# Kernel optimization log

Measured on AMD Instinct MI355X. Metric: run time of the kernel, lower is better.

The kernel has to match this reference:

```python
import jax, jax.numpy as jnp
import numpy as np
from jax import lax

V, H, B, S, N, E = 32000, 128, 8, 512, 50000, 600000


def lstm(x, W_ih, W_hh, b):
    # x: [B,T,D]; W_ih: [4H,D]; W_hh: [4H,H]; b: [4H] (b_ih+b_hh combined)
    Bsz = x.shape[0]
    Hd = W_hh.shape[1]
    xg = jnp.einsum('btd,gd->btg', x, W_ih) + b  # precompute input gates [B,T,4H]
    h0 = jnp.zeros((Bsz, Hd), x.dtype)
    c0 = jnp.zeros((Bsz, Hd), x.dtype)

    def step(carry, g_t):
        h, c = carry
        g = g_t + h @ W_hh.T
        i, f, gg, o = jnp.split(g, 4, axis=-1)
        i = jax.nn.sigmoid(i)
        f = jax.nn.sigmoid(f)
        gg = jnp.tanh(gg)
        o = jax.nn.sigmoid(o)
        c = f * c + i * gg
        h = o * jnp.tanh(c)
        return (h, c), h

    _, hs = lax.scan(step, (h0, c0), jnp.swapaxes(xg, 0, 1))
    return jnp.swapaxes(hs, 0, 1)  # [B,T,H]


def gcn_conv(x, W, b, src, dst, n_nodes):
    # PyG GCNConv: add self-loops, symmetric normalization, out = A_hat (x W) + b
    h = x @ W.T  # [N,H]
    deg = jax.ops.segment_sum(jnp.ones(src.shape[0], x.dtype), dst, num_segments=n_nodes) + 1.0
    dinv = lax.rsqrt(deg)
    norm = dinv[src] * dinv[dst]  # [E]
    agg = jax.ops.segment_sum(h[src] * norm[:, None], dst, num_segments=n_nodes)
    agg = agg + h * (dinv * dinv)[:, None]  # self-loop contribution
    return agg + b


def setup_inputs() -> dict:
    key = jax.random.key(0)
    ks = jax.random.split(key, 20)
    s = 0.02
    return {
        'json_input': jax.random.randint(ks[0], (B, S), 0, V, dtype=jnp.int32),
        'node_ids': jax.random.randint(ks[1], (N,), 0, V, dtype=jnp.int32),
        'edge_index': jax.random.randint(ks[2], (2, E), 0, N, dtype=jnp.int32),
        'embedding': jax.random.normal(ks[3], (V, H), jnp.float32) * s,
        'W_ih_enc': jax.random.normal(ks[4], (4 * H, H), jnp.float32) * s,
        'W_hh_enc': jax.random.normal(ks[5], (4 * H, H), jnp.float32) * s,
        'b_enc': jnp.zeros((4 * H,), jnp.float32),
        'W1': jax.random.normal(ks[6], (H, H), jnp.float32) * s,
        'b1': jnp.zeros((H,), jnp.float32),
        'W2': jax.random.normal(ks[7], (H, H), jnp.float32) * s,
        'b2': jnp.zeros((H,), jnp.float32),
        'Wf': jax.random.normal(ks[8], (H, 2 * H), jnp.float32) * s,
        'bf': jnp.zeros((H,), jnp.float32),
        'W_ih_dec': jax.random.normal(ks[9], (4 * H, H), jnp.float32) * s,
        'W_hh_dec': jax.random.normal(ks[10], (4 * H, H), jnp.float32) * s,
        'b_dec': jnp.zeros((4 * H,), jnp.float32),
        'Wo': jax.random.normal(ks[11], (V, H), jnp.float32) * s,
        'bo': jnp.zeros((V,), jnp.float32),
    }


def reference(json_input, node_ids, edge_index, embedding, W_ih_enc, W_hh_enc, b_enc,
              W1, b1, W2, b2, Wf, bf, W_ih_dec, W_hh_dec, b_dec, Wo, bo):
    src, dst = edge_index[0], edge_index[1]
    # sequence branch
    json_emb = embedding[json_input]                      # [B,S,H]
    json_encoded = lstm(json_emb, W_ih_enc, W_hh_enc, b_enc)  # [B,S,H]
    # graph branch
    node_x = embedding[node_ids]                          # [N,H]
    x = gcn_conv(node_x, W1, b1, src, dst, node_ids.shape[0])
    x = gcn_conv(x, W2, b2, src, dst, node_ids.shape[0])
    # fusion
    graph_summary = jnp.broadcast_to(x.mean(axis=0, keepdims=True), (json_encoded.shape[0], x.shape[1]))
    combined = jnp.concatenate([json_encoded.mean(axis=1), graph_summary], axis=1)  # [B,2H]
    fused = combined @ Wf.T + bf                          # [B,H]
    fused_seq = jnp.broadcast_to(fused[:, None, :], (fused.shape[0], json_input.shape[1], fused.shape[1]))
    # decode
    decoded = lstm(fused_seq, W_ih_dec, W_hh_dec, b_dec)  # [B,S,H]
    return decoded @ Wo.T + bo                            # [B,S,V]
```

## Files before the change

kernel.cpp:

```cpp
#include <hip/hip_runtime.h>
#include <hip/hip_bf16.h>
#include <stdint.h>

#define VV 32000
#define HH 128
#define BB 8
#define SS 512
#define NNODE 50000
#define NEDGE 600000

typedef __attribute__((ext_vector_type(8))) short s16x8;
typedef __attribute__((ext_vector_type(4))) float f32x4;

__global__ __launch_bounds__(256) void xg_enc_kernel(
    const int* __restrict__ jin, const float* __restrict__ emb,
    const float* __restrict__ Wih, const float* __restrict__ bvec,
    float* __restrict__ xg)
{
  __shared__ __align__(16) float arow[8][128];
  const int tid = threadIdx.x, blk = blockIdx.x;
  {
    int r = tid >> 5, c = (tid & 31) << 2;
    int tok = jin[blk*8 + r];
    *(float4*)&arow[r][c] = *(const float4*)&emb[(size_t)tok*HH + c];
  }
  __syncthreads();
  const int g0 = tid * 2;
  const float* w0 = Wih + (size_t)g0*HH;
  const float* w1 = w0 + HH;
  float acc0[8], acc1[8];
  #pragma unroll
  for (int r=0;r<8;r++){ acc0[r]=0.f; acc1[r]=0.f; }
  for (int k=0;k<HH;k+=4) {
    float4 wa = *(const float4*)&w0[k];
    float4 wb = *(const float4*)&w1[k];
    #pragma unroll
    for (int r=0;r<8;r++) {
      float4 av = *(const float4*)&arow[r][k];
      acc0[r] += av.x*wa.x + av.y*wa.y + av.z*wa.z + av.w*wa.w;
      acc1[r] += av.x*wb.x + av.y*wb.y + av.z*wb.z + av.w*wb.w;
    }
  }
  float bb0 = bvec[g0], bb1 = bvec[g0+1];
  #pragma unroll
  for (int r=0;r<8;r++) {
    size_t row = (size_t)blk*8 + r;
    xg[row*512 + g0]     = acc0[r] + bb0;
    xg[row*512 + g0 + 1] = acc1[r] + bb1;
  }
}

__global__ __launch_bounds__(512, 2) void enc_scan_kernel(
    const float* __restrict__ xg, const float* __restrict__ Whh,
    float* __restrict__ hmean)
{
  __shared__ __align__(16) float h_s[128];
  __shared__ float act_s[512];
  const int b = blockIdx.x, tid = threadIdx.x;

  const f32x4* Wrow = (const f32x4*)(Whh + (size_t)tid*HH);
  f32x4 w[32];
  #pragma unroll
  for (int k=0;k<32;k++) w[k] = Wrow[k];
  #pragma unroll
  for (int k=0;k<32;k++) asm volatile("" : "+v"(w[k]));

  const float* xgrow = xg + (size_t)b*SS*512;
  float xv = xgrow[tid];
  if (tid < 128) h_s[tid] = 0.f;
  float cstate = 0.f, hsum = 0.f;
  __syncthreads();

  for (int t=0;t<SS;t++) {
    int tn = (t < SS-1) ? (t+1) : t;
    float nxv = xgrow[(size_t)tn*512 + tid];
    float a0=0.f,a1=0.f,a2=0.f,a3=0.f;
    #pragma unroll
    for (int k=0;k<32;k++) {
      f32x4 hv = *(const f32x4*)&h_s[k*4];
      a0 += w[k].x*hv.x; a1 += w[k].y*hv.y;
      a2 += w[k].z*hv.z; a3 += w[k].w*hv.w;
    }
    float s = (a0+a1)+(a2+a3) + xv;
    int gid = tid >> 7;
    float act = (gid==2) ? tanhf(s) : 1.0f/(1.0f+expf(-s));
    act_s[tid] = act;
    __syncthreads();
    if (tid < 128) {
      float i_ = act_s[tid], f_ = act_s[128+tid], g_ = act_s[256+tid], o_ = act_s[384+tid];
      cstate = f_*cstate + i_*g_;
      float hh = o_*tanhf(cstate);
      h_s[tid] = hh;
      hsum += hh;
    }
    xv = nxv;
    __syncthreads();
  }
  if (tid < 128) hmean[b*HH + tid] = hsum * (1.0f/512.0f);
}

__global__ __launch_bounds__(512) void dec_gemm_kernel(
    const float* __restrict__ xgdec, const float* __restrict__ Whh,
    __hip_bfloat16* __restrict__ ahi, __hip_bfloat16* __restrict__ alo,
    const __hip_bfloat16* __restrict__ Bhi, const __hip_bfloat16* __restrict__ Blo,
    const float* __restrict__ bo, float* __restrict__ out, int* __restrict__ prog)
{
  __shared__ __align__(16) char shraw[131072];
  const int bid = blockIdx.x, tid = threadIdx.x;

  if (bid < 8) {
    float* h_s   = (float*)shraw;
    float* act_s = ((float*)shraw) + 128;
    const int b = bid;

    const f32x4* Wrow = (const f32x4*)(Whh + (size_t)tid*HH);
    f32x4 w[32];
    #pragma unroll
    for (int k=0;k<32;k++) w[k] = Wrow[k];
    #pragma unroll
    for (int k=0;k<32;k++) asm volatile("" : "+v"(w[k]));

    float xv = xgdec[b*512 + tid];
    if (tid < 128) h_s[tid] = 0.f;
    float cstate = 0.f;
    __syncthreads();

    for (int t=0;t<SS;t++) {
      float a0=0.f,a1=0.f,a2=0.f,a3=0.f;
      #pragma unroll
      for (int k=0;k<32;k++) {
        f32x4 hv = *(const f32x4*)&h_s[k*4];
        a0 += w[k].x*hv.x; a1 += w[k].y*hv.y;
        a2 += w[k].z*hv.z; a3 += w[k].w*hv.w;
      }
      float s = (a0+a1)+(a2+a3) + xv;
      int gid = tid >> 7;
      float act = (gid==2) ? tanhf(s) : 1.0f/(1.0f+expf(-s));
      act_s[tid] = act;
      __syncthreads();
      if (tid < 128) {
        float i_ = act_s[tid], f_ = act_s[128+tid], g_ = act_s[256+tid], o_ = act_s[384+tid];
        cstate = f_*cstate + i_*g_;
        float hh = o_*tanhf(cstate);
        h_s[tid] = hh;
        size_t row = (size_t)b*SS + t;
        __hip_bfloat16 hi = __float2bfloat16(hh);
        float rem = hh - __bfloat162float(hi);
        ahi[row*HH + tid] = hi;
        alo[row*HH + tid] = __float2bfloat16(rem);
      }
      __syncthreads();
      if ((t & 127) == 127) {
        __threadfence();
        __syncthreads();
        if (tid == 0)
          __hip_atomic_store(&prog[b*32], (t >> 7) + 1,
                             __ATOMIC_RELEASE, __HIP_MEMORY_SCOPE_AGENT);
      }
    }
  } else {
    short* smem = (short*)shraw;
    const int gbid = bid - 8;
    const int c    = gbid / 1000;
    const int r    = gbid % 1000;
    const int b    = r / 125;
    const int nblk = r % 125;
    const int mtile = b*4 + c;

    if (tid == 0) {
      while (__hip_atomic_load(&prog[b*32], __ATOMIC_ACQUIRE,
                               __HIP_MEMORY_SCOPE_AGENT) <= c)
        __builtin_amdgcn_s_sleep(64);
    }
    __syncthreads();

    const short* bsrc[2] = {
      (const short*)Bhi + (size_t)nblk*256*HH,
      (const short*)Blo + (size_t)nblk*256*HH };
    #pragma unroll
    for (int p=0;p<2;p++) {
      #pragma unroll
      for (int it=0; it<8; it++) {
        int off  = it*8192 + tid*16;
        int row  = off >> 8;
        int soff = off ^ ((row & 15) << 4);
        __builtin_amdgcn_global_load_lds(
          (const __attribute__((address_space(1))) void*)((const char*)bsrc[p] + soff),
          (__attribute__((address_space(3))) void*)((char*)smem + p*65536 + off),
          16, 0, 0);
      }
    }
    __syncthreads();

    const int lane = tid & 63;
    const int wid  = tid >> 6;
    const int wm = wid >> 2, wn = wid & 3;
    const int l15 = lane & 15, l4 = lane >> 4;
    const int mbase = mtile*128 + wm*64;
    const short* Ah = (const short*)ahi;
    const short* Al = (const short*)alo;

    f32x4 acc[4][4] = {};
    #pragma unroll
    for (int s=0;s<4;s++) {
      s16x8 bh[4], bl[4], ah[4], al[4];
      #pragma unroll
      for (int qn=0;qn<4;qn++) {
        int rb   = wn*64 + qn*16 + l15;
        int offb = (rb*256 + s*64 + l4*16) ^ ((rb & 15) << 4);
        bh[qn] = *(const s16x8*)((const char*)smem + offb);
        bl[qn] = *(const s16x8*)((const char*)smem + 65536 + offb);
      }
      #pragma unroll
      for (int qm=0;qm<4;qm++) {
        int arow = mbase + qm*16 + l15;
        size_t aoff = (size_t)arow*HH + s*32 + l4*8;
        ah[qm] = *(const s16x8*)(Ah + aoff);
        al[qm] = *(const s16x8*)(Al + aoff);
      }
      #pragma unroll
      for (int qm=0;qm<4;qm++) {
        #pragma unroll
        for (int qn=0;qn<4;qn++) {
          acc[qm][qn] = __builtin_amdgcn_mfma_f32_16x16x32_bf16(bh[qn], ah[qm], acc[qm][qn], 0,0,0);
          acc[qm][qn] = __builtin_amdgcn_mfma_f32_16x16x32_bf16(bl[qn], ah[qm], acc[qm][qn], 0,0,0);
          acc[qm][qn] = __builtin_amdgcn_mfma_f32_16x16x32_bf16(bh[qn], al[qm], acc[qm][qn], 0,0,0);
        }
      }
    }
    #pragma unroll
    for (int qm=0;qm<4;qm++) {
      int row = mbase + qm*16 + l15;
      #pragma unroll
      for (int qn=0;qn<4;qn++) {
        int colb = nblk*256 + wn*64 + qn*16 + l4*4;
        f32x4 bv = *(const f32x4*)&bo[colb];
        f32x4 o = acc[qm][qn] + bv;
        *(f32x4*)&out[(size_t)row*VV + colb] = o;
      }
    }
  }
}

__global__ __launch_bounds__(256) void edge_deg_kernel(const int* __restrict__ dst, float* __restrict__ deg) {
  int i = blockIdx.x*256 + threadIdx.x;
  if (i < NEDGE) atomicAdd(&deg[dst[i]], 1.0f);
}
__global__ __launch_bounds__(256) void node_dinv_kernel(const float* __restrict__ deg, float* __restrict__ dinv) {
  int n = blockIdx.x*256 + threadIdx.x;
  if (n < NNODE) dinv[n] = 1.0f / sqrtf(deg[n] + 1.0f);
}
__global__ __launch_bounds__(256) void edge_s1_kernel(const int* __restrict__ src, const int* __restrict__ dst,
    const float* __restrict__ dinv, float* __restrict__ s1) {
  int i = blockIdx.x*256 + threadIdx.x;
  if (i < NEDGE) atomicAdd(&s1[src[i]], dinv[dst[i]]);
}
__global__ __launch_bounds__(256) void node_c_kernel(const float* __restrict__ dinv, const float* __restrict__ s1,
    float* __restrict__ cc, float* __restrict__ csum) {
  __shared__ float red[256];
  int tid = threadIdx.x;
  int n = blockIdx.x*256 + tid;
  float v = 0.f;
  if (n < NNODE) { float d = dinv[n]; v = d*s1[n] + d*d; cc[n] = v; }
  red[tid] = v; __syncthreads();
  for (int sfl=128; sfl>0; sfl>>=1) { if (tid < sfl) red[tid] += red[tid+sfl]; __syncthreads(); }
  if (tid==0) atomicAdd(csum, red[0]);
}
__global__ __launch_bounds__(256) void edge_s2_kernel(const int* __restrict__ src, const int* __restrict__ dst,
    const float* __restrict__ dinv, const float* __restrict__ cc, float* __restrict__ s2) {
  int i = blockIdx.x*256 + threadIdx.x;
  if (i < NEDGE) { int d = dst[i]; atomicAdd(&s2[src[i]], cc[d]*dinv[d]); }
}
__global__ __launch_bounds__(256) void node_e_kernel(const float* __restrict__ dinv, const float* __restrict__ s2,
    const float* __restrict__ cc, float* __restrict__ ee) {
  int n = blockIdx.x*256 + threadIdx.x;
  if (n < NNODE) { float d = dinv[n]; ee[n] = d*s2[n] + cc[n]*d*d; }
}
__global__ __launch_bounds__(256) void gvec_kernel(const int* __restrict__ nids, const float* __restrict__ emb,
    const float* __restrict__ ee, float* __restrict__ gvec) {
  __shared__ float red[256];
  int tid = threadIdx.x;
  int j = tid & 127, sub = tid >> 7;
  float acc = 0.f;
  for (int n = blockIdx.x*2 + sub; n < NNODE; n += gridDim.x*2) {
    acc += ee[n] * emb[(size_t)nids[n]*HH + j];
  }
  red[tid] = acc; __syncthreads();
  if (tid < 128) atomicAdd(&gvec[j], red[tid] + red[tid+128]);
}
__global__ void graph_final_kernel(const float* __restrict__ gvec, const float* __restrict__ csum,
    const float* __restrict__ W1, const float* __restrict__ b1,
    const float* __restrict__ W2, const float* __restrict__ b2, float* __restrict__ mvec) {
  __shared__ float gs[128], v1[128];
  int j = threadIdx.x;
  gs[j] = gvec[j];
  __syncthreads();
  float a = 0.f;
  for (int k=0;k<128;k++) a += gs[k]*W1[j*128+k];
  v1[j] = a + csum[0]*b1[j];
  __syncthreads();
  float a2 = 0.f;
  for (int k=0;k<128;k++) a2 += v1[k]*W2[j*128+k];
  mvec[j] = a2 * (1.0f/(float)NNODE) + b2[j];
}

__global__ __launch_bounds__(512) void fusion_kernel(const float* __restrict__ hmean, const float* __restrict__ mvec,
    const float* __restrict__ Wf, const float* __restrict__ bfv,
    const float* __restrict__ Wihd, const float* __restrict__ bd, float* __restrict__ xgdec)
{
  __shared__ float comb[256];
  __shared__ float fus[128];
  int b = blockIdx.x, tid = threadIdx.x;
  if (tid < 128) comb[tid] = hmean[b*128 + tid];
  else if (tid < 256) comb[tid] = mvec[tid - 128];
  __syncthreads();
  if (tid < 128) {
    float a = 0.f;
    for (int k=0;k<256;k++) a += comb[k]*Wf[tid*256+k];
    fus[tid] = a + bfv[tid];
  }
  __syncthreads();
  float a = 0.f;
  for (int k=0;k<128;k++) a += fus[k]*Wihd[tid*128+k];
  xgdec[b*512 + tid] = a + bd[tid];
}

__global__ __launch_bounds__(256) void split_bf16_kernel(const float* __restrict__ x,
    __hip_bfloat16* __restrict__ hi, __hip_bfloat16* __restrict__ lo, int n4) {
  int i = blockIdx.x*256 + threadIdx.x;
  if (i >= n4) return;
  float4 v = *(const float4*)&x[i*4];
  float vv[4] = {v.x, v.y, v.z, v.w};
  #pragma unroll
  for (int k=0;k<4;k++) {
    __hip_bfloat16 h = __float2bfloat16(vv[k]);
    hi[i*4+k] = h;
    lo[i*4+k] = __float2bfloat16(vv[k] - __bfloat162float(h));
  }
}

extern "C" void kernel_launch(void* const* d_in, const int* in_sizes, int n_in,
                              void* d_out, int out_size, void* d_ws, size_t ws_size,
                              hipStream_t stream)
{
  (void)in_sizes; (void)n_in; (void)out_size; (void)ws_size;
  const int*   jin   = (const int*)d_in[0];
  const int*   nids  = (const int*)d_in[1];
  const int*   esrc  = (const int*)d_in[2];
  const int*   edst  = esrc + NEDGE;
  const float* emb   = (const float*)d_in[3];
  const float* WihE  = (const float*)d_in[4];
  const float* WhhE  = (const float*)d_in[5];
  const float* bE    = (const float*)d_in[6];
  const float* W1    = (const float*)d_in[7];
  const float* b1    = (const float*)d_in[8];
  const float* W2    = (const float*)d_in[9];
  const float* b2    = (const float*)d_in[10];
  const float* Wf    = (const float*)d_in[11];
  const float* bfv   = (const float*)d_in[12];
  const float* WihD  = (const float*)d_in[13];
  const float* WhhD  = (const float*)d_in[14];
  const float* bD    = (const float*)d_in[15];
  const float* Wo    = (const float*)d_in[16];
  const float* bo    = (const float*)d_in[17];
  float* out = (float*)d_out;

  char* ws = (char*)d_ws;
  size_t off = 0;
  auto alloc = [&](size_t bytes) { size_t o = off; off = (off + bytes + 255) & ~(size_t)255; return o; };

  int*   prog = (int*)(ws + alloc(BB*32*4));
  float* deg  = (float*)(ws + alloc(NNODE*4));
  float* s1   = (float*)(ws + alloc(NNODE*4));
  float* s2   = (float*)(ws + alloc(NNODE*4));
  float* gvec = (float*)(ws + alloc(128*4));
  float* csum = (float*)(ws + alloc(4));
  size_t zero_bytes = off;
  float* dinv = (float*)(ws + alloc(NNODE*4));
  float* cc   = (float*)(ws + alloc(NNODE*4));
  float* ee   = (float*)(ws + alloc(NNODE*4));
  float* mvec = (float*)(ws + alloc(128*4));
  float* hmean= (float*)(ws + alloc(BB*HH*4));
  float* xgdec= (float*)(ws + alloc(BB*512*4));
  float* xgenc= (float*)(ws + alloc((size_t)BB*SS*512*4));
  __hip_bfloat16* Ahi = (__hip_bfloat16*)(ws + alloc((size_t)BB*SS*HH*2));
  __hip_bfloat16* Alo = (__hip_bfloat16*)(ws + alloc((size_t)BB*SS*HH*2));
  __hip_bfloat16* Bhi = (__hip_bfloat16*)(ws + alloc((size_t)VV*HH*2));
  __hip_bfloat16* Blo = (__hip_bfloat16*)(ws + alloc((size_t)VV*HH*2));

  hipMemsetAsync(ws, 0, zero_bytes, stream);

  split_bf16_kernel<<<dim3((VV*HH/4+255)/256), dim3(256), 0, stream>>>(Wo, Bhi, Blo, VV*HH/4);

  xg_enc_kernel<<<dim3((BB*SS)/8), dim3(256), 0, stream>>>(jin, emb, WihE, bE, xgenc);
  enc_scan_kernel<<<dim3(BB), dim3(512), 0, stream>>>(xgenc, WhhE, hmean);

  edge_deg_kernel<<<dim3((NEDGE+255)/256), dim3(256), 0, stream>>>(edst, deg);
  node_dinv_kernel<<<dim3((NNODE+255)/256), dim3(256), 0, stream>>>(deg, dinv);
  edge_s1_kernel<<<dim3((NEDGE+255)/256), dim3(256), 0, stream>>>(esrc, edst, dinv, s1);
  node_c_kernel<<<dim3((NNODE+255)/256), dim3(256), 0, stream>>>(dinv, s1, cc, csum);
  edge_s2_kernel<<<dim3((NEDGE+255)/256), dim3(256), 0, stream>>>(esrc, edst, dinv, cc, s2);
  node_e_kernel<<<dim3((NNODE+255)/256), dim3(256), 0, stream>>>(dinv, s2, cc, ee);
  gvec_kernel<<<dim3(256), dim3(256), 0, stream>>>(nids, emb, ee, gvec);
  graph_final_kernel<<<dim3(1), dim3(128), 0, stream>>>(gvec, csum, W1, b1, W2, b2, mvec);

  fusion_kernel<<<dim3(BB), dim3(512), 0, stream>>>(hmean, mvec, Wf, bfv, WihD, bD, xgdec);
  dec_gemm_kernel<<<dim3(8 + 4000), dim3(512), 0, stream>>>(
      xgdec, WhhD, Ahi, Alo, Bhi, Blo, bo, out, prog);
}
```

Baseline: 1.284 ms.

## Fuse front-end kernels into one persistent kernel overlapping encoder scan with graph work

Replaces the encoder input-gate GEMM, encoder scan, Wo bf16 split and all GCN reduction kernels with one persistent launch. Eight blocks run the encoder scans while 240 worker blocks produce xg chunks, signalled through per-chunk counters, then do the bf16 split and graph stages separated by a software grid barrier. This overlaps the serial scan with the parallel work and removes many launches. The decoder GEMM also drops to 64-row M tiles with progress flags every 64 steps so projection starts earlier, at the cost of twice as many blocks. The software grid barrier relies on all 248 blocks being co-resident, which is a deadlock risk if they are not.

```diff
diff --git a/kernel.cpp b/kernel.cpp
--- a/kernel.cpp
+++ b/kernel.cpp
@@ -8,95 +8,198 @@
 #define SS 512
 #define NNODE 50000
 #define NEDGE 600000
+#define NWORK 240
 
 typedef __attribute__((ext_vector_type(8))) short s16x8;
 typedef __attribute__((ext_vector_type(4))) float f32x4;
 
-__global__ __launch_bounds__(256) void xg_enc_kernel(
-    const int* __restrict__ jin, const float* __restrict__ emb,
-    const float* __restrict__ Wih, const float* __restrict__ bvec,
-    float* __restrict__ xg)
-{
-  __shared__ __align__(16) float arow[8][128];
-  const int tid = threadIdx.x, blk = blockIdx.x;
-  {
-    int r = tid >> 5, c = (tid & 31) << 2;
-    int tok = jin[blk*8 + r];
-    *(float4*)&arow[r][c] = *(const float4*)&emb[(size_t)tok*HH + c];
+__device__ __forceinline__ void workers_barrier(int* bar, int tid) {
+  __syncthreads();
+  if (tid == 0) {
+    int g = __hip_atomic_load(&bar[32], __ATOMIC_ACQUIRE, __HIP_MEMORY_SCOPE_AGENT);
+    int old = __hip_atomic_fetch_add(&bar[0], 1, __ATOMIC_ACQ_REL, __HIP_MEMORY_SCOPE_AGENT);
+    if (old == NWORK-1) {
+      __hip_atomic_store(&bar[0], 0, __ATOMIC_RELAXED, __HIP_MEMORY_SCOPE_AGENT);
+      __hip_atomic_store(&bar[32], g+1, __ATOMIC_RELEASE, __HIP_MEMORY_SCOPE_AGENT);
+    } else {
+      while (__hip_atomic_load(&bar[32], __ATOMIC_ACQUIRE, __HIP_MEMORY_SCOPE_AGENT) == g)
+        __builtin_amdgcn_s_sleep(32);
+    }
   }
   __syncthreads();
-  const int g0 = tid * 2;
-  const float* w0 = Wih + (size_t)g0*HH;
-  const float* w1 = w0 + HH;
-  float acc0[8], acc1[8];
-  #pragma unroll
-  for (int r=0;r<8;r++){ acc0[r]=0.f; acc1[r]=0.f; }
-  for (int k=0;k<HH;k+=4) {
-    float4 wa = *(const float4*)&w0[k];
-    float4 wb = *(const float4*)&w1[k];
-    #pragma unroll
-    for (int r=0;r<8;r++) {
-      float4 av = *(const float4*)&arow[r][k];
-      acc0[r] += av.x*wa.x + av.y*wa.y + av.z*wa.z + av.w*wa.w;
-      acc1[r] += av.x*wb.x + av.y*wb.y + av.z*wb.z + av.w*wb.w;
+}
+
+__global__ __launch_bounds__(512) void front_kernel(
+    const int* __restrict__ jin, const float* __restrict__ emb,
+    const float* __restrict__ WihE, const float* __restrict__ bE,
+    float* xg, const float* __restrict__ WhhE, float* __restrict__ hmean,
+    const float* __restrict__ Wo, __hip_bfloat16* __restrict__ Bhi, __hip_bfloat16* __restrict__ Blo,
+    const int* __restrict__ esrc, const int* __restrict__ edst, const int* __restrict__ nids,
+    float* __restrict__ deg, float* __restrict__ dinv, float* __restrict__ s1,
+    float* __restrict__ s2, float* __restrict__ cc, float* __restrict__ ee,
+    float* __restrict__ csum, float* __restrict__ gvec,
+    const float* __restrict__ W1, const float* __restrict__ b1,
+    const float* __restrict__ W2, const float* __restrict__ b2, float* __restrict__ mvec,
+    int* ucnt, int* bar)
+{
+  __shared__ __align__(16) char shraw[131072];
+  const int bid = blockIdx.x, tid = threadIdx.x;
+
+  if (bid < 8) {
+    float* h_s   = (float*)shraw;
+    float* act_s = ((float*)shraw) + 128;
+    const int b = bid;
+
+    const f32x4* Wrow = (const f32x4*)(WhhE + (size_t)tid*HH);
+    f32x4 w[32];
+    #pragma unroll
+    for (int k=0;k<32;k++) w[k] = Wrow[k];
+    #pragma unroll
+    for (int k=0;k<32;k++) asm volatile("" : "+v"(w[k]));
+
+    const float* xgrow = xg + (size_t)b*SS*512;
+    if (tid == 0) {
+      while (__hip_atomic_load(&ucnt[(b*8+0)*32], __ATOMIC_ACQUIRE, __HIP_MEMORY_SCOPE_AGENT) < 8)
+        __builtin_amdgcn_s_sleep(16);
+    }
+    __syncthreads();
+    float xv = xgrow[tid];
+    if (tid < 128) h_s[tid] = 0.f;
+    float cstate = 0.f, hsum = 0.f;
+    __syncthreads();
+
+    for (int t=0;t<SS;t++) {
+      if ((t & 63) == 0) {
+        int cn = (t >> 6) + 1; if (cn > 7) cn = 7;
+        if (tid == 0) {
+          while (__hip_atomic_load(&ucnt[(b*8+cn)*32], __ATOMIC_ACQUIRE, __HIP_MEMORY_SCOPE_AGENT) < 8)
+            __builtin_amdgcn_s_sleep(16);
+        }
+        __syncthreads();
+      }
+      int tn = (t < SS-1) ? (t+1) : t;
+      float nxv = xgrow[(size_t)tn*512 + tid];
+      float a0=0.f,a1=0.f,a2=0.f,a3=0.f;
+      #pragma unroll
+      for (int k=0;k<32;k++) {
+        f32x4 hv = *(const f32x4*)&h_s[k*4];
+        a0 += w[k].x*hv.x; a1 += w[k].y*hv.y;
+        a2 += w[k].z*hv.z; a3 += w[k].w*hv.w;
+      }
+      float s = (a0+a1)+(a2+a3) + xv;
+      int gid = tid >> 7;
+      float act = (gid==2) ? tanhf(s) : 1.0f/(1.0f+expf(-s));
+      act_s[tid] = act;
+      __syncthreads();
+      if (tid < 128) {
+        float i_ = act_s[tid], f_ = act_s[128+tid], g_ = act_s[256+tid], o_ = act_s[384+tid];
+        cstate = f_*cstate + i_*g_;
+        float hh = o_*tanhf(cstate);
+        h_s[tid] = hh;
+        hsum += hh;
+      }
+      xv = nxv;
+      __syncthreads();
+    }
+    if (tid < 128) hmean[b*HH + tid] = hsum * (1.0f/512.0f);
+  } else {
+    const int wbid = bid - 8;
+    float (*arow)[128] = (float(*)[128])shraw;
+    float* red = (float*)(shraw + 8*128*4);
+
+    for (int u = wbid; u < 512; u += NWORK) {
+      int c = u >> 6, r2 = u & 63, b = r2 >> 3, sub = r2 & 7;
+      int row0 = b*512 + c*64 + sub*8;
+      if (tid < 256) {
+        int r = tid >> 5, c4 = (tid & 31) << 2;
+        int tok = jin[row0 + r];
+        *(float4*)&arow[r][c4] = *(const float4*)&emb[(size_t)tok*HH + c4];
+      }
+      __syncthreads();
+      const float* w0 = WihE + (size_t)tid*HH;
+      float acc[8];
+      #pragma unroll
+      for (int r=0;r<8;r++) acc[r] = 0.f;
+      for (int k=0;k<HH;k+=4) {
+        float4 wa = *(const float4*)&w0[k];
+        #pragma unroll
+        for (int r=0;r<8;r++) {
+          float4 av = *(const float4*)&arow[r][k];
+          acc[r] += av.x*wa.x + av.y*wa.y + av.z*wa.z + av.w*wa.w;
+        }
+      }
+      float bb = bE[tid];
+      #pragma unroll
+      for (int r=0;r<8;r++)
+        xg[(size_t)(row0+r)*512 + tid] = acc[r] + bb;
+      __threadfence();
+      __syncthreads();
+      if (tid == 0)
+        __hip_atomic_fetch_add(&ucnt[(b*8+c)*32], 1, __ATOMIC_RELEASE, __HIP_MEMORY_SCOPE_AGENT);
+      __syncthreads();
+    }
+    for (int i = wbid*512 + tid; i < VV*HH/4; i += NWORK*512) {
+      float4 v = *(const float4*)&Wo[i*4];
+      float vv[4] = {v.x, v.y, v.z, v.w};
+      #pragma unroll
+      for (int k=0;k<4;k++) {
+        __hip_bfloat16 h = __float2bfloat16(vv[k]);
+        Bhi[i*4+k] = h;
+        Blo[i*4+k] = __float2bfloat16(vv[k] - __bfloat162float(h));
+      }
+    }
+    workers_barrier(bar, tid);
+    for (int i = wbid*512 + tid; i < NEDGE; i += NWORK*512)
+      atomicAdd(&deg[edst[i]], 1.0f);
+    workers_barrier(bar, tid);
+    for (int n = wbid*512 + tid; n < NNODE; n += NWORK*512)
+      dinv[n] = 1.0f / sqrtf(deg[n] + 1.0f);
+    workers_barrier(bar, tid);
+    for (int i = wbid*512 + tid; i < NEDGE; i += NWORK*512)
+      atomicAdd(&s1[esrc[i]], dinv[edst[i]]);
+    workers_barrier(bar, tid);
+    {
+      float lsum = 0.f;
+      for (int n = wbid*512 + tid; n < NNODE; n += NWORK*512) {
+        float d = dinv[n]; float v = d*s1[n] + d*d; cc[n] = v; lsum += v;
+      }
+      red[tid] = lsum; __syncthreads();
+      for (int sfl=256; sfl>0; sfl>>=1) { if (tid < sfl) red[tid] += red[tid+sfl]; __syncthreads(); }
+      if (tid==0) atomicAdd(csum, red[0]);
+    }
+    workers_barrier(bar, tid);
+    for (int i = wbid*512 + tid; i < NEDGE; i += NWORK*512) {
+      int d = edst[i]; atomicAdd(&s2[esrc[i]], cc[d]*dinv[d]);
+    }
+    workers_barrier(bar, tid);
+    for (int n = wbid*512 + tid; n < NNODE; n += NWORK*512) {
+      float d = dinv[n]; ee[n] = d*s2[n] + cc[n]*d*d;
+    }
+    workers_barrier(bar, tid);
+    {
+      int j = tid & 127, sub = tid >> 7;
+      float acc = 0.f;
+      for (int n = wbid*4 + sub; n < NNODE; n += NWORK*4)
+        acc += ee[n] * emb[(size_t)nids[n]*HH + j];
+      red[tid] = acc; __syncthreads();
+      if (tid < 128) atomicAdd(&gvec[j], red[tid] + red[tid+128] + red[tid+256] + red[tid+384]);
+    }
+    workers_barrier(bar, tid);
+    if (wbid == 0 && tid < 128) {
+      float* gs = (float*)shraw;
+      float* v1 = gs + 128;
+      int j = tid;
+      gs[j] = gvec[j];
+      __builtin_amdgcn_s_barrier();
+      float a = 0.f;
+      for (int k=0;k<128;k++) a += gs[k]*W1[j*128+k];
+      v1[j] = a + csum[0]*b1[j];
+      __builtin_amdgcn_s_barrier();
+      float a2 = 0.f;
+      for (int k=0;k<128;k++) a2 += v1[k]*W2[j*128+k];
+      mvec[j] = a2 * (1.0f/(float)NNODE) + b2[j];
     }
   }
-  float bb0 = bvec[g0], bb1 = bvec[g0+1];
-  #pragma unroll
-  for (int r=0;r<8;r++) {
-    size_t row = (size_t)blk*8 + r;
-    xg[row*512 + g0]     = acc0[r] + bb0;
-    xg[row*512 + g0 + 1] = acc1[r] + bb1;
-  }
-}
-
-__global__ __launch_bounds__(512, 2) void enc_scan_kernel(
-    const float* __restrict__ xg, const float* __restrict__ Whh,
-    float* __restrict__ hmean)
-{
-  __shared__ __align__(16) float h_s[128];
-  __shared__ float act_s[512];
-  const int b = blockIdx.x, tid = threadIdx.x;
-
-  const f32x4* Wrow = (const f32x4*)(Whh + (size_t)tid*HH);
-  f32x4 w[32];
-  #pragma unroll
-  for (int k=0;k<32;k++) w[k] = Wrow[k];
-  #pragma unroll
-  for (int k=0;k<32;k++) asm volatile("" : "+v"(w[k]));
-
-  const float* xgrow = xg + (size_t)b*SS*512;
-  float xv = xgrow[tid];
-  if (tid < 128) h_s[tid] = 0.f;
-  float cstate = 0.f, hsum = 0.f;
-  __syncthreads();
-
-  for (int t=0;t<SS;t++) {
-    int tn = (t < SS-1) ? (t+1) : t;
-    float nxv = xgrow[(size_t)tn*512 + tid];
-    float a0=0.f,a1=0.f,a2=0.f,a3=0.f;
-    #pragma unroll
-    for (int k=0;k<32;k++) {
-      f32x4 hv = *(const f32x4*)&h_s[k*4];
-      a0 += w[k].x*hv.x; a1 += w[k].y*hv.y;
-      a2 += w[k].z*hv.z; a3 += w[k].w*hv.w;
-    }
-    float s = (a0+a1)+(a2+a3) + xv;
-    int gid = tid >> 7;
-    float act = (gid==2) ? tanhf(s) : 1.0f/(1.0f+expf(-s));
-    act_s[tid] = act;
-    __syncthreads();
-    if (tid < 128) {
-      float i_ = act_s[tid], f_ = act_s[128+tid], g_ = act_s[256+tid], o_ = act_s[384+tid];
-      cstate = f_*cstate + i_*g_;
-      float hh = o_*tanhf(cstate);
-      h_s[tid] = hh;
-      hsum += hh;
-    }
-    xv = nxv;
-    __syncthreads();
-  }
-  if (tid < 128) hmean[b*HH + tid] = hsum * (1.0f/512.0f);
 }
 
 __global__ __launch_bounds__(512) void dec_gemm_kernel(
@@ -150,11 +253,11 @@
         alo[row*HH + tid] = __float2bfloat16(rem);
       }
       __syncthreads();
-      if ((t & 127) == 127) {
+      if ((t & 63) == 63) {
         __threadfence();
         __syncthreads();
         if (tid == 0)
-          __hip_atomic_store(&prog[b*32], (t >> 7) + 1,
+          __hip_atomic_store(&prog[b*32], (t >> 6) + 1,
                              __ATOMIC_RELEASE, __HIP_MEMORY_SCOPE_AGENT);
       }
     }
@@ -165,7 +268,7 @@
     const int r    = gbid % 1000;
     const int b    = r / 125;
     const int nblk = r % 125;
-    const int mtile = b*4 + c;
+    const int mbase0 = b*512 + c*64;
 
     if (tid == 0) {
       while (__hip_atomic_load(&prog[b*32], __ATOMIC_ACQUIRE,
@@ -196,14 +299,14 @@
     const int wid  = tid >> 6;
     const int wm = wid >> 2, wn = wid & 3;
     const int l15 = lane & 15, l4 = lane >> 4;
-    const int mbase = mtile*128 + wm*64;
+    const int mbase = mbase0 + wm*32;
     const short* Ah = (const short*)ahi;
     const short* Al = (const short*)alo;
 
-    f32x4 acc[4][4] = {};
+    f32x4 acc[2][4] = {};
     #pragma unroll
     for (int s=0;s<4;s++) {
-      s16x8 bh[4], bl[4], ah[4], al[4];
+      s16x8 bh[4], bl[4], ah[2], al[2];
       #pragma unroll
       for (int qn=0;qn<4;qn++) {
         int rb   = wn*64 + qn*16 + l15;
@@ -212,14 +315,14 @@
         bl[qn] = *(const s16x8*)((const char*)smem + 65536 + offb);
       }
       #pragma unroll
-      for (int qm=0;qm<4;qm++) {
+      for (int qm=0;qm<2;qm++) {
         int arow = mbase + qm*16 + l15;
         size_t aoff = (size_t)arow*HH + s*32 + l4*8;
         ah[qm] = *(const s16x8*)(Ah + aoff);
         al[qm] = *(const s16x8*)(Al + aoff);
       }
       #pragma unroll
-      for (int qm=0;qm<4;qm++) {
+      for (int qm=0;qm<2;qm++) {
         #pragma unroll
         for (int qn=0;qn<4;qn++) {
           acc[qm][qn] = __builtin_amdgcn_mfma_f32_16x16x32_bf16(bh[qn], ah[qm], acc[qm][qn], 0,0,0);
@@ -229,7 +332,7 @@
       }
     }
     #pragma unroll
-    for (int qm=0;qm<4;qm++) {
+    for (int qm=0;qm<2;qm++) {
       int row = mbase + qm*16 + l15;
       #pragma unroll
       for (int qn=0;qn<4;qn++) {
@@ -240,68 +343,6 @@
       }
     }
   }
-}
-
-__global__ __launch_bounds__(256) void edge_deg_kernel(const int* __restrict__ dst, float* __restrict__ deg) {
-  int i = blockIdx.x*256 + threadIdx.x;
-  if (i < NEDGE) atomicAdd(&deg[dst[i]], 1.0f);
-}
-__global__ __launch_bounds__(256) void node_dinv_kernel(const float* __restrict__ deg, float* __restrict__ dinv) {
-  int n = blockIdx.x*256 + threadIdx.x;
-  if (n < NNODE) dinv[n] = 1.0f / sqrtf(deg[n] + 1.0f);
-}
-__global__ __launch_bounds__(256) void edge_s1_kernel(const int* __restrict__ src, const int* __restrict__ dst,
-    const float* __restrict__ dinv, float* __restrict__ s1) {
-  int i = blockIdx.x*256 + threadIdx.x;
-  if (i < NEDGE) atomicAdd(&s1[src[i]], dinv[dst[i]]);
-}
-__global__ __launch_bounds__(256) void node_c_kernel(const float* __restrict__ dinv, const float* __restrict__ s1,
-    float* __restrict__ cc, float* __restrict__ csum) {
-  __shared__ float red[256];
-  int tid = threadIdx.x;
-  int n = blockIdx.x*256 + tid;
-  float v = 0.f;
-  if (n < NNODE) { float d = dinv[n]; v = d*s1[n] + d*d; cc[n] = v; }
-  red[tid] = v; __syncthreads();
-  for (int sfl=128; sfl>0; sfl>>=1) { if (tid < sfl) red[tid] += red[tid+sfl]; __syncthreads(); }
-  if (tid==0) atomicAdd(csum, red[0]);
-}
-__global__ __launch_bounds__(256) void edge_s2_kernel(const int* __restrict__ src, const int* __restrict__ dst,
-    const float* __restrict__ dinv, const float* __restrict__ cc, float* __restrict__ s2) {
-  int i = blockIdx.x*256 + threadIdx.x;
-  if (i < NEDGE) { int d = dst[i]; atomicAdd(&s2[src[i]], cc[d]*dinv[d]); }
-}
-__global__ __launch_bounds__(256) void node_e_kernel(const float* __restrict__ dinv, const float* __restrict__ s2,
-    const float* __restrict__ cc, float* __restrict__ ee) {
-  int n = blockIdx.x*256 + threadIdx.x;
-  if (n < NNODE) { float d = dinv[n]; ee[n] = d*s2[n] + cc[n]*d*d; }
-}
-__global__ __launch_bounds__(256) void gvec_kernel(const int* __restrict__ nids, const float* __restrict__ emb,
-    const float* __restrict__ ee, float* __restrict__ gvec) {
-  __shared__ float red[256];
-  int tid = threadIdx.x;
-  int j = tid & 127, sub = tid >> 7;
-  float acc = 0.f;
-  for (int n = blockIdx.x*2 + sub; n < NNODE; n += gridDim.x*2) {
-    acc += ee[n] * emb[(size_t)nids[n]*HH + j];
-  }
-  red[tid] = acc; __syncthreads();
-  if (tid < 128) atomicAdd(&gvec[j], red[tid] + red[tid+128]);
-}
-__global__ void graph_final_kernel(const float* __restrict__ gvec, const float* __restrict__ csum,
-    const float* __restrict__ W1, const float* __restrict__ b1,
-    const float* __restrict__ W2, const float* __restrict__ b2, float* __restrict__ mvec) {
-  __shared__ float gs[128], v1[128];
-  int j = threadIdx.x;
-  gs[j] = gvec[j];
-  __syncthreads();
-  float a = 0.f;
-  for (int k=0;k<128;k++) a += gs[k]*W1[j*128+k];
-  v1[j] = a + csum[0]*b1[j];
-  __syncthreads();
-  float a2 = 0.f;
-  for (int k=0;k<128;k++) a2 += v1[k]*W2[j*128+k];
-  mvec[j] = a2 * (1.0f/(float)NNODE) + b2[j];
 }
 
 __global__ __launch_bounds__(512) void fusion_kernel(const float* __restrict__ hmean, const float* __restrict__ mvec,
@@ -323,20 +364,6 @@
   float a = 0.f;
   for (int k=0;k<128;k++) a += fus[k]*Wihd[tid*128+k];
   xgdec[b*512 + tid] = a + bd[tid];
-}
-
-__global__ __launch_bounds__(256) void split_bf16_kernel(const float* __restrict__ x,
-    __hip_bfloat16* __restrict__ hi, __hip_bfloat16* __restrict__ lo, int n4) {
-  int i = blockIdx.x*256 + threadIdx.x;
-  if (i >= n4) return;
-  float4 v = *(const float4*)&x[i*4];
-  float vv[4] = {v.x, v.y, v.z, v.w};
-  #pragma unroll
-  for (int k=0;k<4;k++) {
-    __hip_bfloat16 h = __float2bfloat16(vv[k]);
-    hi[i*4+k] = h;
-    lo[i*4+k] = __float2bfloat16(vv[k] - __bfloat162float(h));
-  }
 }
 
 extern "C" void kernel_launch(void* const* d_in, const int* in_sizes, int n_in,
@@ -370,6 +397,8 @@
   auto alloc = [&](size_t bytes) { size_t o = off; off = (off + bytes + 255) & ~(size_t)255; return o; };
 
   int*   prog = (int*)(ws + alloc(BB*32*4));
+  int*   ucnt = (int*)(ws + alloc(BB*8*32*4));
+  int*   bar  = (int*)(ws + alloc(64*4));
   float* deg  = (float*)(ws + alloc(NNODE*4));
   float* s1   = (float*)(ws + alloc(NNODE*4));
   float* s2   = (float*)(ws + alloc(NNODE*4));
@@ -390,21 +419,12 @@
 
   hipMemsetAsync(ws, 0, zero_bytes, stream);
 
-  split_bf16_kernel<<<dim3((VV*HH/4+255)/256), dim3(256), 0, stream>>>(Wo, Bhi, Blo, VV*HH/4);
-
-  xg_enc_kernel<<<dim3((BB*SS)/8), dim3(256), 0, stream>>>(jin, emb, WihE, bE, xgenc);
-  enc_scan_kernel<<<dim3(BB), dim3(512), 0, stream>>>(xgenc, WhhE, hmean);
-
-  edge_deg_kernel<<<dim3((NEDGE+255)/256), dim3(256), 0, stream>>>(edst, deg);
-  node_dinv_kernel<<<dim3((NNODE+255)/256), dim3(256), 0, stream>>>(deg, dinv);
-  edge_s1_kernel<<<dim3((NEDGE+255)/256), dim3(256), 0, stream>>>(esrc, edst, dinv, s1);
-  node_c_kernel<<<dim3((NNODE+255)/256), dim3(256), 0, stream>>>(dinv, s1, cc, csum);
-  edge_s2_kernel<<<dim3((NEDGE+255)/256), dim3(256), 0, stream>>>(esrc, edst, dinv, cc, s2);
-  node_e_kernel<<<dim3((NNODE+255)/256), dim3(256), 0, stream>>>(dinv, s2, cc, ee);
-  gvec_kernel<<<dim3(256), dim3(256), 0, stream>>>(nids, emb, ee, gvec);
-  graph_final_kernel<<<dim3(1), dim3(128), 0, stream>>>(gvec, csum, W1, b1, W2, b2, mvec);
+  front_kernel<<<dim3(8 + NWORK), dim3(512), 0, stream>>>(
+      jin, emb, WihE, bE, xgenc, WhhE, hmean, Wo, Bhi, Blo,
+      esrc, edst, nids, deg, dinv, s1, s2, cc, ee, csum, gvec,
+      W1, b1, W2, b2, mvec, ucnt, bar);
 
   fusion_kernel<<<dim3(BB), dim3(512), 0, stream>>>(hmean, mvec, Wf, bfv, WihD, bD, xgdec);
-  dec_gemm_kernel<<<dim3(8 + 4000), dim3(512), 0, stream>>>(
+  dec_gemm_kernel<<<dim3(8 + 8000), dim3(512), 0, stream>>>(
       xgdec, WhhD, Ahi, Alo, Bhi, Blo, bo, out, prog);
 }
```

Result: faster. 1.252 ms (-2.5%).
